# Optimization experiments

Measured on AMD Instinct MI355X. Metric: run time of the kernel, lower is better.

The kernel has to match this reference:

```python
import jax, jax.numpy as jnp
import numpy as np

N_NODES = 100000
N_EDGES = 1600000
IN_DIM = 128
HID = 128
Z_DIM = 16
NUM_LAYERS = 3


def gcn_conv(x, W, b, src, dst, num_nodes):
    """PyG-style GCNConv with self-loops and symmetric normalization.
    src/dst already include self-loops. x: [N, Fin], W: [Fin, Fout]."""
    xw = x @ W  # [N, Fout]
    deg = jax.ops.segment_sum(jnp.ones(src.shape[0], dtype=x.dtype), dst,
                              num_segments=num_nodes)  # >=1 due to self-loops
    dinv = jax.lax.rsqrt(jnp.maximum(deg, 1.0))
    norm = dinv[src] * dinv[dst]  # [E]
    msg = xw[src] * norm[:, None]  # [E, Fout] gather
    out = jax.ops.segment_sum(msg, dst, num_segments=num_nodes)  # scatter-add
    return out + b


def setup_inputs() -> dict:
    key = jax.random.key(0)
    ks = jax.random.split(key, 10)
    adj = jax.random.randint(ks[0], (2, N_EDGES), 0, N_NODES, dtype=jnp.int32)
    X = jax.random.normal(ks[1], (N_NODES, IN_DIM), dtype=jnp.float32)
    s = 0.05
    fc1_W = jax.random.normal(ks[2], (IN_DIM, 128), dtype=jnp.float32) * s
    fc1_b = jnp.zeros((128,), dtype=jnp.float32)
    fc2_W = jax.random.normal(ks[3], (128, HID), dtype=jnp.float32) * s
    fc2_b = jnp.zeros((HID,), dtype=jnp.float32)
    gcn_W = jax.random.normal(ks[4], (NUM_LAYERS, HID, HID), dtype=jnp.float32) * s
    gcn_b = jnp.zeros((NUM_LAYERS, HID), dtype=jnp.float32)
    assign_W = jax.random.normal(ks[5], (HID, Z_DIM), dtype=jnp.float32) * s
    assign_b = jnp.zeros((Z_DIM,), dtype=jnp.float32)
    return {"adj": adj, "X": X, "fc1_W": fc1_W, "fc1_b": fc1_b,
            "fc2_W": fc2_W, "fc2_b": fc2_b, "gcn_W": gcn_W, "gcn_b": gcn_b,
            "assign_W": assign_W, "assign_b": assign_b}


def reference(adj, X, fc1_W, fc1_b, fc2_W, fc2_b, gcn_W, gcn_b, assign_W, assign_b):
    n = X.shape[0]
    loop = jnp.arange(n, dtype=adj.dtype)
    src = jnp.concatenate([adj[0], loop])  # add self-loops
    dst = jnp.concatenate([adj[1], loop])
    h = jax.nn.sigmoid(X @ fc1_W + fc1_b)
    h = jax.nn.sigmoid(h @ fc2_W + fc2_b)
    for i in range(NUM_LAYERS):
        h = gcn_conv(h, gcn_W[i], gcn_b[i], src, dst, n)
    assign = gcn_conv(h, assign_W, assign_b, src, dst, n)
    return assign
```

## Files before the change

kernel.cpp:

```cpp
#include <hip/hip_runtime.h>
#include <cstdint>
#include <cstddef>


#define SCAN_CHUNK 2048

typedef _Float16 half8 __attribute__((ext_vector_type(8)));
typedef float floatx4 __attribute__((ext_vector_type(4)));

__global__ __launch_bounds__(256) void scan_partial_k(const int* __restrict__ cnt, int N,
                                                      int* __restrict__ bsum) {
  __shared__ int red[256];
  int b = blockIdx.x, t = threadIdx.x;
  int base = b * SCAN_CHUNK + t * 8;
  int s = 0;
#pragma unroll
  for (int i = 0; i < 8; ++i) {
    int idx = base + i;
    if (idx < N) s += cnt[idx];
  }
  red[t] = s;
  __syncthreads();
  for (int off = 128; off > 0; off >>= 1) {
    if (t < off) red[t] += red[t + off];
    __syncthreads();
  }
  if (t == 0) bsum[b] = red[0];
}

__global__ __launch_bounds__(64) void scan_bsum_k(int* __restrict__ bsum, int NB) {
  int lane = threadIdx.x;
  int per = (NB + 63) >> 6;
  int beg = lane * per;
  int end = min(beg + per, NB);
  int s = 0;
  for (int i = beg; i < end; ++i) s += bsum[i];
  int ps = s;
  for (int off = 1; off < 64; off <<= 1) {
    int u = __shfl_up(ps, off, 64);
    if (lane >= off) ps += u;
  }
  int run = ps - s;
  for (int i = beg; i < end; ++i) {
    int c = bsum[i];
    bsum[i] = run;
    run += c;
  }
}

__global__ __launch_bounds__(256) void scan_apply_k(const int* __restrict__ cnt,
                                                    const int* __restrict__ bsum_excl, int N,
                                                    int* __restrict__ rowptr,
                                                    int* __restrict__ cursor, int E) {
  __shared__ int wave_sums[4];
  int b = blockIdx.x, t = threadIdx.x;
  int base = b * SCAN_CHUNK + t * 8;
  int v[8];
  int s = 0;
#pragma unroll
  for (int i = 0; i < 8; ++i) {
    int idx = base + i;
    v[i] = (idx < N) ? cnt[idx] : 0;
    s += v[i];
  }
  int lane = t & 63, wave = t >> 6;
  int ps = s;
  for (int off = 1; off < 64; off <<= 1) {
    int u = __shfl_up(ps, off, 64);
    if (lane >= off) ps += u;
  }
  if (lane == 63) wave_sums[wave] = ps;
  __syncthreads();
  int woff = 0;
  for (int w = 0; w < 4; ++w)
    if (w < wave) woff += wave_sums[w];
  int excl = woff + (ps - s) + bsum_excl[b];
#pragma unroll
  for (int i = 0; i < 8; ++i) {
    int idx = base + i;
    if (idx < N) {
      rowptr[idx] = excl;
      cursor[idx] = excl;
      excl += v[i];
    }
  }
  if (b == 0 && t == 0) rowptr[N] = E;
}

__global__ __launch_bounds__(256) void p1a_hist_k(const int* __restrict__ dst, int E, int G,
                                                  int B, int chunk, int* __restrict__ M) {
  __shared__ int h[256];
  int g = blockIdx.x, t = threadIdx.x;
  for (int i = t; i < B; i += 256) h[i] = 0;
  __syncthreads();
  int ebeg = g * chunk, eend = min(ebeg + chunk, E);
  for (int e = ebeg + t; e < eend; e += 256) atomicAdd(&h[dst[e] >> 9], 1);
  __syncthreads();
  for (int b = t; b < B; b += 256) M[(size_t)b * G + g] = h[b];
}

__global__ __launch_bounds__(256) void p1c_scatter_k(const int* __restrict__ src,
                                                     const int* __restrict__ dst, int E, int G,
                                                     int B, int chunk,
                                                     const int* __restrict__ scanned,
                                                     uint32_t* __restrict__ tmp) {
  __shared__ int off[256];
  int g = blockIdx.x, t = threadIdx.x;
  for (int b = t; b < B; b += 256) off[b] = scanned[(size_t)b * G + g];
  __syncthreads();
  int ebeg = g * chunk, eend = min(ebeg + chunk, E);
  for (int e = ebeg + t; e < eend; e += 256) {
    int d = dst[e];
    int b = d >> 9;
    int pos = atomicAdd(&off[b], 1);
    tmp[pos] = ((uint32_t)(d & 511) << 17) | (uint32_t)src[e];
  }
}

__global__ __launch_bounds__(256) void p2_build_k(const uint32_t* __restrict__ tmp,
                                                  const int* __restrict__ scanned, int G, int N,
                                                  int E, int* __restrict__ rowptr,
                                                  int* __restrict__ col,
                                                  float* __restrict__ dinv,
                                                  float* __restrict__ dinv2) {
  __shared__ int hist[512];
  __shared__ int cur[512];
  __shared__ int wsum[4];
  int b = blockIdx.x, t = threadIdx.x;
  int node0 = b << 9;
  int nn = min(512, N - node0);
  int sbeg = scanned[(size_t)b * G];
  int send = scanned[(size_t)(b + 1) * G];
  for (int i = t; i < 512; i += 256) hist[i] = 0;
  __syncthreads();
  for (int e = sbeg + t; e < send; e += 256) atomicAdd(&hist[tmp[e] >> 17], 1);
  __syncthreads();
  int h0 = hist[2 * t], h1 = hist[2 * t + 1];
  int s = h0 + h1;
  int lane = t & 63, w = t >> 6;
  int ps = s;
  for (int o = 1; o < 64; o <<= 1) {
    int u = __shfl_up(ps, o, 64);
    if (lane >= o) ps += u;
  }
  if (lane == 63) wsum[w] = ps;
  __syncthreads();
  int woff = 0;
  for (int k = 0; k < 4; ++k)
    if (k < w) woff += wsum[k];
  int excl = sbeg + woff + (ps - s);
  if (2 * t < nn) {
    rowptr[node0 + 2 * t] = excl;
    cur[2 * t] = excl;
    dinv[node0 + 2 * t] = rsqrtf((float)(h0 + 1));
    dinv2[node0 + 2 * t] = 1.f / (float)(h0 + 1);
  }
  if (2 * t + 1 < nn) {
    rowptr[node0 + 2 * t + 1] = excl + h0;
    cur[2 * t + 1] = excl + h0;
    dinv[node0 + 2 * t + 1] = rsqrtf((float)(h1 + 1));
    dinv2[node0 + 2 * t + 1] = 1.f / (float)(h1 + 1);
  }
  if (b == 0 && t == 0) rowptr[N] = E;
  __syncthreads();
  for (int e = sbeg + t; e < send; e += 256) {
    uint32_t u = tmp[e];
    int pos = atomicAdd(&cur[u >> 17], 1);
    col[pos] = (int)(u & 0x1FFFF);
  }
}

__global__ __launch_bounds__(256) void count_edges_k(const int* __restrict__ dst, int E,
                                                     int* __restrict__ cnt) {
  int idx = blockIdx.x * blockDim.x + threadIdx.x;
  int stride = gridDim.x * blockDim.x;
  for (int e = idx; e < E; e += stride) atomicAdd(&cnt[dst[e]], 1);
}

__global__ __launch_bounds__(256) void dinv_k(const int* __restrict__ cnt,
                                              float* __restrict__ dinv,
                                              float* __restrict__ dinv2, int N) {
  int i = blockIdx.x * blockDim.x + threadIdx.x;
  if (i < N) {
    dinv[i] = rsqrtf((float)(cnt[i] + 1));
    dinv2[i] = 1.f / (float)(cnt[i] + 1);
  }
}

__global__ __launch_bounds__(256) void fill_k(const int* __restrict__ src,
                                              const int* __restrict__ dst, int E,
                                              int* __restrict__ cursor, int* __restrict__ col) {
  int idx = blockIdx.x * blockDim.x + threadIdx.x;
  int stride = gridDim.x * blockDim.x;
  for (int e = idx; e < E; e += stride) {
    int d = dst[e];
    int pos = atomicAdd(&cursor[d], 1);
    col[pos] = src[e];
  }
}

__global__ __launch_bounds__(256) void wprep_k(const float* __restrict__ fc1_W,
                                               const float* __restrict__ fc2_W,
                                               _Float16* __restrict__ Wb) {
  int idx = blockIdx.x * 256 + threadIdx.x;
  if (idx < 2 * 16384) {
    int mat = idx >> 14;
    int r = idx & 16383;
    int t = r >> 11;
    int ktb = (r >> 9) & 3;
    int lane = (r >> 3) & 63;
    int j = r & 7;
    int m = lane & 15, q = lane >> 4;
    int k = ktb * 32 + q * 8 + j;
    int n = t * 16 + m;
    const float* W = (mat == 0) ? fc1_W : fc2_W;
    Wb[idx] = (_Float16)W[(size_t)k * 128 + n];
  }
}

__global__ __launch_bounds__(256) void chain_mm_k(const float* __restrict__ A,
                                                  const float* __restrict__ B,
                                                  float* __restrict__ C) {
  __shared__ float Bl[2048];
  int t = threadIdx.x;
  for (int i = t; i < 2048; i += 256) Bl[i] = B[i];
  __syncthreads();
  int idx = blockIdx.x * 256 + t;
  int row = idx >> 4, f = idx & 15;
  const float* Ar = A + (size_t)row * 128;
  float s = 0.f;
#pragma unroll 8
  for (int j = 0; j < 128; ++j) s = fmaf(Ar[j], Bl[j * 16 + f], s);
  C[idx] = s;
}

__global__ __launch_bounds__(256) void chain_frag_k(const float* __restrict__ W0,
                                                    const float* __restrict__ T1,
                                                    const float* __restrict__ T2,
                                                    const float* __restrict__ assign_W,
                                                    const float* __restrict__ gcn_b,
                                                    _Float16* __restrict__ WbT,
                                                    float* __restrict__ cvec) {
  int t = threadIdx.x;
  if (blockIdx.x < 8) {
    __shared__ float T1l[2048];
    for (int i = t; i < 2048; i += 256) T1l[i] = T1[i];
    __syncthreads();
    int idx = blockIdx.x * 256 + t;
    int ktb = idx >> 9;
    int lane = (idx >> 3) & 63;
    int jj = idx & 7;
    int m = lane & 15, qq = lane >> 4;
    int k = ktb * 32 + qq * 8 + jj;
    const float* Ar = W0 + (size_t)k * 128;
    float s = 0.f;
#pragma unroll 8
    for (int j = 0; j < 128; ++j) s = fmaf(Ar[j], T1l[j * 16 + m], s);
    WbT[idx] = (_Float16)s;
  } else {
    if (t < 16) {
      float s3 = 0.f, s2 = 0.f, s1 = 0.f;
      for (int k = 0; k < 128; ++k) {
        s3 += gcn_b[k] * T1[k * 16 + t];
        s2 += gcn_b[128 + k] * T2[k * 16 + t];
        s1 += gcn_b[256 + k] * assign_W[k * 16 + t];
      }
      cvec[t] = s3;
      cvec[16 + t] = s2;
      cvec[32 + t] = s1;
    }
  }
}

__global__ __launch_bounds__(256) void mlp_fused_k(const float* __restrict__ X,
                                                   const _Float16* __restrict__ Wb,
                                                   const float* __restrict__ fc1_b,
                                                   const float* __restrict__ fc2_b,
                                                   const _Float16* __restrict__ WbT,
                                                   const float* __restrict__ dinv,
                                                   _Float16* __restrict__ S, int N) {
  __shared__ _Float16 Wst[16384];
  __shared__ _Float16 hl[4][16 * 136];
  const int tid = threadIdx.x;
  const int w = tid >> 6, lane = tid & 63;
  const int m = lane & 15, q = lane >> 4;
  const int r0 = (blockIdx.x * 4 + w) * 16;
  const int rowA = r0 + m;
  const bool validA = rowA < N;
  _Float16* hw = hl[w];

  float4 xa[8];
#pragma unroll
  for (int ktb = 0; ktb < 4; ++ktb) {
    if (validA) {
      const float* Ap = X + (size_t)rowA * 128 + ktb * 32 + q * 8;
      xa[2 * ktb] = *(const float4*)Ap;
      xa[2 * ktb + 1] = *(const float4*)(Ap + 4);
    } else {
      xa[2 * ktb] = (float4){0.f, 0.f, 0.f, 0.f};
      xa[2 * ktb + 1] = (float4){0.f, 0.f, 0.f, 0.f};
    }
  }
  {
    half8 v[8];
#pragma unroll
    for (int i = 0; i < 8; ++i) v[i] = *(const half8*)(Wb + ((size_t)(i * 256 + tid)) * 8);
#pragma unroll
    for (int i = 0; i < 8; ++i) *(half8*)(Wst + (size_t)(i * 256 + tid) * 8) = v[i];
  }
  __syncthreads();

  floatx4 acc[8];
#pragma unroll
  for (int t = 0; t < 8; ++t) acc[t] = (floatx4){0.f, 0.f, 0.f, 0.f};
#pragma unroll
  for (int ktb = 0; ktb < 4; ++ktb) {
    half8 a;
    float4 f0 = xa[2 * ktb], f1 = xa[2 * ktb + 1];
    a[0] = (_Float16)f0.x; a[1] = (_Float16)f0.y;
    a[2] = (_Float16)f0.z; a[3] = (_Float16)f0.w;
    a[4] = (_Float16)f1.x; a[5] = (_Float16)f1.y;
    a[6] = (_Float16)f1.z; a[7] = (_Float16)f1.w;
#pragma unroll
    for (int t = 0; t < 8; ++t) {
      half8 b = *(const half8*)(Wst + ((size_t)(t * 4 + ktb) * 64 + lane) * 8);
      acc[t] = __builtin_amdgcn_mfma_f32_16x16x32_f16(a, b, acc[t], 0, 0, 0);
    }
  }
#pragma unroll
  for (int t = 0; t < 8; ++t) {
    int colg = t * 16 + m;
    float bz = fc1_b[colg];
#pragma unroll
    for (int r = 0; r < 4; ++r) {
      float v = acc[t][r] + bz;
      v = 1.f / (1.f + __expf(-v));
      hw[(q * 4 + r) * 136 + colg] = (_Float16)v;
    }
  }
  __syncthreads();
  {
    const _Float16* Wb2 = Wb + 16384;
    half8 v[8];
#pragma unroll
    for (int i = 0; i < 8; ++i) v[i] = *(const half8*)(Wb2 + ((size_t)(i * 256 + tid)) * 8);
#pragma unroll
    for (int i = 0; i < 8; ++i) *(half8*)(Wst + (size_t)(i * 256 + tid) * 8) = v[i];
  }
  __syncthreads();

#pragma unroll
  for (int t = 0; t < 8; ++t) acc[t] = (floatx4){0.f, 0.f, 0.f, 0.f};
#pragma unroll
  for (int ktb = 0; ktb < 4; ++ktb) {
    half8 a = *(const half8*)(hw + m * 136 + ktb * 32 + q * 8);
#pragma unroll
    for (int t = 0; t < 8; ++t) {
      half8 b = *(const half8*)(Wst + ((size_t)(t * 4 + ktb) * 64 + lane) * 8);
      acc[t] = __builtin_amdgcn_mfma_f32_16x16x32_f16(a, b, acc[t], 0, 0, 0);
    }
  }
#pragma unroll
  for (int t = 0; t < 8; ++t) {
    int colg = t * 16 + m;
    float bz = fc2_b[colg];
#pragma unroll
    for (int r = 0; r < 4; ++r) {
      float v = acc[t][r] + bz;
      v = 1.f / (1.f + __expf(-v));
      hw[(q * 4 + r) * 136 + colg] = (_Float16)v;
    }
  }
  floatx4 p0 = (floatx4){0.f, 0.f, 0.f, 0.f};
#pragma unroll
  for (int ktb = 0; ktb < 4; ++ktb) {
    half8 a = *(const half8*)(hw + m * 136 + ktb * 32 + q * 8);
    half8 b = *(const half8*)(WbT + ((size_t)ktb * 64 + lane) * 8);
    p0 = __builtin_amdgcn_mfma_f32_16x16x32_f16(a, b, p0, 0, 0, 0);
  }
#pragma unroll
  for (int r = 0; r < 4; ++r) {
    int row = r0 + q * 4 + r;
    if (row < N) S[(size_t)row * 16 + m] = (_Float16)(p0[r] * dinv[row]);
  }
}

template <bool FOUT32>
__global__ __launch_bounds__(256) void agg16q_k(const _Float16* __restrict__ xw,
                                                const int* __restrict__ rowptr,
                                                const int* __restrict__ col,
                                                const float* __restrict__ rowscale,
                                                const float* __restrict__ biasmul,
                                                const float* __restrict__ c,
                                                void* __restrict__ outv, int N) {
  int w = blockIdx.x * 4 + (threadIdx.x >> 6);
  int n0 = w * 4;
  if (n0 >= N) return;
  int lane = threadIdx.x & 63;
  int f = lane & 15;
  int j = lane >> 4;
  int b0 = rowptr[n0];
  int s1 = rowptr[min(n0 + 1, N)];
  int s2 = rowptr[min(n0 + 2, N)];
  int s3 = rowptr[min(n0 + 3, N)];
  int e4 = rowptr[min(n0 + 4, N)];
  int D = e4 - b0;
  int q = (D + 3) >> 2;
  int e = b0 + j * q;
  int ee = min(e + q, e4);
  float p0 = 0.f, p1 = 0.f, p2 = 0.f, p3 = 0.f;
  for (; e + 7 < ee; e += 8) {
    int cc[8];
#pragma unroll
    for (int i = 0; i < 8; ++i) cc[i] = col[e + i];
    float vv[8];
#pragma unroll
    for (int i = 0; i < 8; ++i) vv[i] = (float)xw[(size_t)cc[i] * 16 + f];
#pragma unroll
    for (int i = 0; i < 8; ++i) {
      int ei = e + i;
      float v = vv[i];
      p0 += (ei < s1) ? v : 0.f;
      p1 += (ei < s2) ? v : 0.f;
      p2 += (ei < s3) ? v : 0.f;
      p3 += v;
    }
  }
  for (; e < ee; ++e) {
    float v = (float)xw[(size_t)col[e] * 16 + f];
    p0 += (e < s1) ? v : 0.f;
    p1 += (e < s2) ? v : 0.f;
    p2 += (e < s3) ? v : 0.f;
    p3 += v;
  }
  p0 += __shfl_xor(p0, 16, 64);
  p0 += __shfl_xor(p0, 32, 64);
  p1 += __shfl_xor(p1, 16, 64);
  p1 += __shfl_xor(p1, 32, 64);
  p2 += __shfl_xor(p2, 16, 64);
  p2 += __shfl_xor(p2, 32, 64);
  p3 += __shfl_xor(p3, 16, 64);
  p3 += __shfl_xor(p3, 32, 64);
  float mine = (j == 0) ? p0 : (j == 1) ? (p1 - p0) : (j == 2) ? (p2 - p1) : (p3 - p2);
  int nj = n0 + j;
  if (nj < N) {
    float a = mine + (float)xw[(size_t)nj * 16 + f];
    float bm = biasmul ? biasmul[nj] : 1.f;
    float o = fmaf(a, rowscale[nj], bm * c[f]);
    if (FOUT32)
      ((float*)outv)[(size_t)nj * 16 + f] = o;
    else
      ((_Float16*)outv)[(size_t)nj * 16 + f] = (_Float16)o;
  }
}

extern "C" void kernel_launch(void* const* d_in, const int* in_sizes, int n_in,
                              void* d_out, int out_size, void* d_ws, size_t ws_size,
                              hipStream_t stream) {
  const int* adj = (const int*)d_in[0];
  const float* X = (const float*)d_in[1];
  const float* fc1_W = (const float*)d_in[2];
  const float* fc1_b = (const float*)d_in[3];
  const float* fc2_W = (const float*)d_in[4];
  const float* fc2_b = (const float*)d_in[5];
  const float* gcn_W = (const float*)d_in[6];
  const float* gcn_b = (const float*)d_in[7];
  const float* assign_W = (const float*)d_in[8];
  const float* assign_b = (const float*)d_in[9];
  const int E = in_sizes[0] / 2;
  const int N = in_sizes[1] / 128;
  const int* src = adj;
  const int* dst = adj + E;

  char* ws = (char*)d_ws;
  size_t off = 0;
  auto alloc = [&](size_t bytes) {
    void* p = ws + off;
    off = (off + bytes + 511) & ~(size_t)511;
    return p;
  };
  const int G = 256;
  const int B = (N + 511) >> 9;
  const int L = B * G;
  _Float16* SA = (_Float16*)alloc((size_t)N * 16 * 2);
  _Float16* SB = (_Float16*)alloc((size_t)N * 16 * 2);
  _Float16* Wb = (_Float16*)alloc((size_t)2 * 16384 * 2);
  _Float16* WbT = (_Float16*)alloc(2048 * 2);
  float* T2g = (float*)alloc(2048 * 4);
  float* T1g = (float*)alloc(2048 * 4);
  float* cvec = (float*)alloc(48 * 4);
  float* dinv = (float*)alloc((size_t)N * 4);
  float* dinv2 = (float*)alloc((size_t)N * 4);
  int* rowptr = (int*)alloc((size_t)(N + 1) * 4);
  int* col = (int*)alloc((size_t)E * 4);
  uint32_t* tmp = (uint32_t*)alloc((size_t)E * 4);
  int* M = (int*)alloc((size_t)L * 4);
  int* scanned = (int*)alloc((size_t)(L + 1) * 4);
  int* scanscratch = (int*)alloc((size_t)L * 4);
  int* bsum = (int*)alloc(4096);
  int* cnt = (int*)alloc((size_t)N * 4);
  int* cursor = (int*)alloc((size_t)N * 4);

  wprep_k<<<(2 * 16384 + 255) / 256, 256, 0, stream>>>(fc1_W, fc2_W, Wb);
  chain_mm_k<<<8, 256, 0, stream>>>(gcn_W + 32768, assign_W, T2g);
  chain_mm_k<<<8, 256, 0, stream>>>(gcn_W + 16384, T2g, T1g);
  chain_frag_k<<<9, 256, 0, stream>>>(gcn_W, T1g, T2g, assign_W, gcn_b, WbT, cvec);

  if (N <= (1 << 17)) {
    const int chunk = (E + G - 1) / G;
    const int NBL = (L + SCAN_CHUNK - 1) / SCAN_CHUNK;
    p1a_hist_k<<<G, 256, 0, stream>>>(dst, E, G, B, chunk, M);
    scan_partial_k<<<NBL, 256, 0, stream>>>(M, L, bsum);
    scan_bsum_k<<<1, 64, 0, stream>>>(bsum, NBL);
    scan_apply_k<<<NBL, 256, 0, stream>>>(M, bsum, L, scanned, scanscratch, E);
    p1c_scatter_k<<<G, 256, 0, stream>>>(src, dst, E, G, B, chunk, scanned, tmp);
    p2_build_k<<<B, 256, 0, stream>>>(tmp, scanned, G, N, E, rowptr, col, dinv, dinv2);
  } else {
    const int NB = (N + SCAN_CHUNK - 1) / SCAN_CHUNK;
    hipMemsetAsync(cnt, 0, (size_t)N * 4, stream);
    count_edges_k<<<2048, 256, 0, stream>>>(dst, E, cnt);
    dinv_k<<<(N + 255) / 256, 256, 0, stream>>>(cnt, dinv, dinv2, N);
    scan_partial_k<<<NB, 256, 0, stream>>>(cnt, N, bsum);
    scan_bsum_k<<<1, 64, 0, stream>>>(bsum, NB);
    scan_apply_k<<<NB, 256, 0, stream>>>(cnt, bsum, N, rowptr, cursor, E);
    fill_k<<<2048, 256, 0, stream>>>(src, dst, E, cursor, col);
  }

  int gfuse = (N + 63) / 64;
  int ab = (N + 15) / 16;
  mlp_fused_k<<<gfuse, 256, 0, stream>>>(X, Wb, fc1_b, fc2_b, WbT, dinv, SA, N);
  agg16q_k<false><<<ab, 256, 0, stream>>>(SA, rowptr, col, dinv2, dinv, cvec, SB, N);
  agg16q_k<false><<<ab, 256, 0, stream>>>(SB, rowptr, col, dinv2, dinv, cvec + 16, SA, N);
  agg16q_k<false><<<ab, 256, 0, stream>>>(SA, rowptr, col, dinv2, dinv, cvec + 32, SB, N);
  agg16q_k<true><<<ab, 256, 0, stream>>>(SB, rowptr, col, dinv, nullptr, assign_b,
                                         (float*)d_out, N);
}
```

Before: 304.2 us.

## Make fused MLP kernel persistent with weights held in registers

Replaces the per-64-row MLP kernel, which restaged both 128x128 fp16 weight matrices into LDS in every block, with a persistent kernel of up to 768 blocks. Each block loops over 16-row tiles, and each wave keeps its 32-column slice of both weight matrices plus the projection weights in registers, so weights are loaded once per block. The four waves now split the output columns of one tile rather than each owning its own rows. The cost is that every wave re-reads and converts the same X rows, the final 16-wide projection is computed redundantly by all four waves, and each tile adds two block barriers.

```diff
diff --git a/kernel.cpp b/kernel.cpp
--- a/kernel.cpp
+++ b/kernel.cpp
@@ -272,116 +272,110 @@
   }
 }
 
-__global__ __launch_bounds__(256) void mlp_fused_k(const float* __restrict__ X,
-                                                   const _Float16* __restrict__ Wb,
-                                                   const float* __restrict__ fc1_b,
-                                                   const float* __restrict__ fc2_b,
-                                                   const _Float16* __restrict__ WbT,
-                                                   const float* __restrict__ dinv,
-                                                   _Float16* __restrict__ S, int N) {
-  __shared__ _Float16 Wst[16384];
-  __shared__ _Float16 hl[4][16 * 136];
+__global__ __launch_bounds__(256) void mlp_pers_k(const float* __restrict__ X,
+                                                  const _Float16* __restrict__ Wb,
+                                                  const float* __restrict__ fc1_b,
+                                                  const float* __restrict__ fc2_b,
+                                                  const _Float16* __restrict__ WbT,
+                                                  const float* __restrict__ dinv,
+                                                  _Float16* __restrict__ S, int N,
+                                                  int ntiles) {
+  __shared__ _Float16 hA[16 * 136];
+  __shared__ _Float16 hB[16 * 136];
   const int tid = threadIdx.x;
   const int w = tid >> 6, lane = tid & 63;
   const int m = lane & 15, q = lane >> 4;
-  const int r0 = (blockIdx.x * 4 + w) * 16;
-  const int rowA = r0 + m;
-  const bool validA = rowA < N;
-  _Float16* hw = hl[w];
-
-  float4 xa[8];
-#pragma unroll
-  for (int ktb = 0; ktb < 4; ++ktb) {
-    if (validA) {
-      const float* Ap = X + (size_t)rowA * 128 + ktb * 32 + q * 8;
-      xa[2 * ktb] = *(const float4*)Ap;
-      xa[2 * ktb + 1] = *(const float4*)(Ap + 4);
-    } else {
-      xa[2 * ktb] = (float4){0.f, 0.f, 0.f, 0.f};
-      xa[2 * ktb + 1] = (float4){0.f, 0.f, 0.f, 0.f};
-    }
-  }
-  {
-    half8 v[8];
-#pragma unroll
-    for (int i = 0; i < 8; ++i) v[i] = *(const half8*)(Wb + ((size_t)(i * 256 + tid)) * 8);
-#pragma unroll
-    for (int i = 0; i < 8; ++i) *(half8*)(Wst + (size_t)(i * 256 + tid) * 8) = v[i];
-  }
-  __syncthreads();
-
-  floatx4 acc[8];
-#pragma unroll
-  for (int t = 0; t < 8; ++t) acc[t] = (floatx4){0.f, 0.f, 0.f, 0.f};
-#pragma unroll
-  for (int ktb = 0; ktb < 4; ++ktb) {
-    half8 a;
-    float4 f0 = xa[2 * ktb], f1 = xa[2 * ktb + 1];
-    a[0] = (_Float16)f0.x; a[1] = (_Float16)f0.y;
-    a[2] = (_Float16)f0.z; a[3] = (_Float16)f0.w;
-    a[4] = (_Float16)f1.x; a[5] = (_Float16)f1.y;
-    a[6] = (_Float16)f1.z; a[7] = (_Float16)f1.w;
-#pragma unroll
-    for (int t = 0; t < 8; ++t) {
-      half8 b = *(const half8*)(Wst + ((size_t)(t * 4 + ktb) * 64 + lane) * 8);
-      acc[t] = __builtin_amdgcn_mfma_f32_16x16x32_f16(a, b, acc[t], 0, 0, 0);
-    }
-  }
-#pragma unroll
-  for (int t = 0; t < 8; ++t) {
-    int colg = t * 16 + m;
-    float bz = fc1_b[colg];
-#pragma unroll
-    for (int r = 0; r < 4; ++r) {
-      float v = acc[t][r] + bz;
-      v = 1.f / (1.f + __expf(-v));
-      hw[(q * 4 + r) * 136 + colg] = (_Float16)v;
-    }
-  }
-  __syncthreads();
-  {
-    const _Float16* Wb2 = Wb + 16384;
-    half8 v[8];
-#pragma unroll
-    for (int i = 0; i < 8; ++i) v[i] = *(const half8*)(Wb2 + ((size_t)(i * 256 + tid)) * 8);
-#pragma unroll
-    for (int i = 0; i < 8; ++i) *(half8*)(Wst + (size_t)(i * 256 + tid) * 8) = v[i];
-  }
-  __syncthreads();
-
-#pragma unroll
-  for (int t = 0; t < 8; ++t) acc[t] = (floatx4){0.f, 0.f, 0.f, 0.f};
-#pragma unroll
-  for (int ktb = 0; ktb < 4; ++ktb) {
-    half8 a = *(const half8*)(hw + m * 136 + ktb * 32 + q * 8);
-#pragma unroll
-    for (int t = 0; t < 8; ++t) {
-      half8 b = *(const half8*)(Wst + ((size_t)(t * 4 + ktb) * 64 + lane) * 8);
-      acc[t] = __builtin_amdgcn_mfma_f32_16x16x32_f16(a, b, acc[t], 0, 0, 0);
-    }
-  }
-#pragma unroll
-  for (int t = 0; t < 8; ++t) {
-    int colg = t * 16 + m;
-    float bz = fc2_b[colg];
-#pragma unroll
-    for (int r = 0; r < 4; ++r) {
-      float v = acc[t][r] + bz;
-      v = 1.f / (1.f + __expf(-v));
-      hw[(q * 4 + r) * 136 + colg] = (_Float16)v;
-    }
-  }
-  floatx4 p0 = (floatx4){0.f, 0.f, 0.f, 0.f};
-#pragma unroll
-  for (int ktb = 0; ktb < 4; ++ktb) {
-    half8 a = *(const half8*)(hw + m * 136 + ktb * 32 + q * 8);
-    half8 b = *(const half8*)(WbT + ((size_t)ktb * 64 + lane) * 8);
-    p0 = __builtin_amdgcn_mfma_f32_16x16x32_f16(a, b, p0, 0, 0, 0);
-  }
-#pragma unroll
-  for (int r = 0; r < 4; ++r) {
-    int row = r0 + q * 4 + r;
-    if (row < N) S[(size_t)row * 16 + m] = (_Float16)(p0[r] * dinv[row]);
+  const _Float16* Wb2 = Wb + 16384;
+
+  half8 b1[2][4], b2[2][4], bt[4];
+#pragma unroll
+  for (int t = 0; t < 2; ++t)
+#pragma unroll
+    for (int ktb = 0; ktb < 4; ++ktb) {
+      b1[t][ktb] = *(const half8*)(Wb + (((size_t)(2 * w + t) * 4 + ktb) * 64 + lane) * 8);
+      b2[t][ktb] = *(const half8*)(Wb2 + (((size_t)(2 * w + t) * 4 + ktb) * 64 + lane) * 8);
+    }
+#pragma unroll
+  for (int ktb = 0; ktb < 4; ++ktb)
+    bt[ktb] = *(const half8*)(WbT + ((size_t)ktb * 64 + lane) * 8);
+  float bz1[2], bz2[2];
+#pragma unroll
+  for (int t = 0; t < 2; ++t) {
+    bz1[t] = fc1_b[(2 * w + t) * 16 + m];
+    bz2[t] = fc2_b[(2 * w + t) * 16 + m];
+  }
+
+  for (int tile = blockIdx.x; tile < ntiles; tile += gridDim.x) {
+    int r0 = tile * 16;
+    int rowA = r0 + m;
+    bool valid = rowA < N;
+    half8 xa[4];
+#pragma unroll
+    for (int ktb = 0; ktb < 4; ++ktb) {
+      half8 a = {0, 0, 0, 0, 0, 0, 0, 0};
+      if (valid) {
+        const float* Ap = X + (size_t)rowA * 128 + ktb * 32 + q * 8;
+        float4 f0 = *(const float4*)Ap;
+        float4 f1 = *(const float4*)(Ap + 4);
+        a[0] = (_Float16)f0.x; a[1] = (_Float16)f0.y;
+        a[2] = (_Float16)f0.z; a[3] = (_Float16)f0.w;
+        a[4] = (_Float16)f1.x; a[5] = (_Float16)f1.y;
+        a[6] = (_Float16)f1.z; a[7] = (_Float16)f1.w;
+      }
+      xa[ktb] = a;
+    }
+    floatx4 acc0 = (floatx4){0.f, 0.f, 0.f, 0.f};
+    floatx4 acc1 = (floatx4){0.f, 0.f, 0.f, 0.f};
+#pragma unroll
+    for (int ktb = 0; ktb < 4; ++ktb) {
+      acc0 = __builtin_amdgcn_mfma_f32_16x16x32_f16(xa[ktb], b1[0][ktb], acc0, 0, 0, 0);
+      acc1 = __builtin_amdgcn_mfma_f32_16x16x32_f16(xa[ktb], b1[1][ktb], acc1, 0, 0, 0);
+    }
+#pragma unroll
+    for (int t = 0; t < 2; ++t) {
+      int colg = (2 * w + t) * 16 + m;
+      float bz = bz1[t];
+#pragma unroll
+      for (int r = 0; r < 4; ++r) {
+        float v = ((t == 0) ? acc0[r] : acc1[r]) + bz;
+        v = 1.f / (1.f + __expf(-v));
+        hA[(q * 4 + r) * 136 + colg] = (_Float16)v;
+      }
+    }
+    __syncthreads();
+    acc0 = (floatx4){0.f, 0.f, 0.f, 0.f};
+    acc1 = (floatx4){0.f, 0.f, 0.f, 0.f};
+#pragma unroll
+    for (int ktb = 0; ktb < 4; ++ktb) {
+      half8 a = *(const half8*)(hA + m * 136 + ktb * 32 + q * 8);
+      acc0 = __builtin_amdgcn_mfma_f32_16x16x32_f16(a, b2[0][ktb], acc0, 0, 0, 0);
+      acc1 = __builtin_amdgcn_mfma_f32_16x16x32_f16(a, b2[1][ktb], acc1, 0, 0, 0);
+    }
+#pragma unroll
+    for (int t = 0; t < 2; ++t) {
+      int colg = (2 * w + t) * 16 + m;
+      float bz = bz2[t];
+#pragma unroll
+      for (int r = 0; r < 4; ++r) {
+        float v = ((t == 0) ? acc0[r] : acc1[r]) + bz;
+        v = 1.f / (1.f + __expf(-v));
+        hB[(q * 4 + r) * 136 + colg] = (_Float16)v;
+      }
+    }
+    __syncthreads();
+    floatx4 p = (floatx4){0.f, 0.f, 0.f, 0.f};
+#pragma unroll
+    for (int ktb = 0; ktb < 4; ++ktb) {
+      half8 a = *(const half8*)(hB + m * 136 + ktb * 32 + q * 8);
+      p = __builtin_amdgcn_mfma_f32_16x16x32_f16(a, bt[ktb], p, 0, 0, 0);
+    }
+    if (w == 0) {
+#pragma unroll
+      for (int r = 0; r < 4; ++r) {
+        int row = r0 + q * 4 + r;
+        if (row < N) S[(size_t)row * 16 + m] = (_Float16)(p[r] * dinv[row]);
+      }
+    }
   }
 }
 
@@ -526,9 +520,10 @@
     fill_k<<<2048, 256, 0, stream>>>(src, dst, E, cursor, col);
   }
 
-  int gfuse = (N + 63) / 64;
+  int ntiles = (N + 15) / 16;
+  int gm = ntiles < 768 ? ntiles : 768;
   int ab = (N + 15) / 16;
-  mlp_fused_k<<<gfuse, 256, 0, stream>>>(X, Wb, fc1_b, fc2_b, WbT, dinv, SA, N);
+  mlp_pers_k<<<gm, 256, 0, stream>>>(X, Wb, fc1_b, fc2_b, WbT, dinv, SA, N, ntiles);
   agg16q_k<false><<<ab, 256, 0, stream>>>(SA, rowptr, col, dinv2, dinv, cvec, SB, N);
   agg16q_k<false><<<ab, 256, 0, stream>>>(SB, rowptr, col, dinv2, dinv, cvec + 16, SA, N);
   agg16q_k<false><<<ab, 256, 0, stream>>>(SA, rowptr, col, dinv2, dinv, cvec + 32, SB, N);
```

Measured after the change: 311.9 us. 1.03x slower.
